# Optimization experiments

Hardware: AMD Instinct MI355X
Metric: run time of the kernel (lower is better)

Reference implementation:

```python
import jax, jax.numpy as jnp
import numpy as np

N, E, D, H, C, L = 100000, 1280000, 64, 4, 16, 3  # nodes, edges, dim, heads, head_dim, layers
NEG_SLOPE = 0.2
LN_EPS = 1e-5


def setup_inputs() -> dict:
    key = jax.random.key(0)
    ks = jax.random.split(key, 6)
    scale = 1.0 / np.sqrt(D)
    x = jax.random.normal(ks[0], (N, D), dtype=jnp.float32)
    edge_index = jax.random.randint(ks[1], (2, E), 0, N, dtype=jnp.int64)
    Wl = jax.random.normal(ks[2], (L, D, H * C), dtype=jnp.float32) * scale  # lin_l (source)
    Wr = jax.random.normal(ks[3], (L, D, H * C), dtype=jnp.float32) * scale  # lin_r (target)
    att = jax.random.normal(ks[4], (L, H, C), dtype=jnp.float32) * scale
    bias = jnp.zeros((L, H * C), dtype=jnp.float32)
    gamma = jnp.ones((L, D), dtype=jnp.float32)
    beta = jnp.zeros((L, D), dtype=jnp.float32)
    return dict(x=x, edge_index=edge_index, Wl=Wl, Wr=Wr, att=att, bias=bias, gamma=gamma, beta=beta)


def _gatv2_conv(x, src, dst, Wl, Wr, att, bias):
    # GATv2Conv (concat=True, share_weights=False, negative_slope=0.2)
    n = x.shape[0]
    xl = (x @ Wl).reshape(n, H, C)  # messages from source nodes
    xr = (x @ Wr).reshape(n, H, C)  # target-side transform
    m = xl[src] + xr[dst]  # [E', H, C]
    e = jnp.einsum('ehc,hc->eh', jax.nn.leaky_relu(m, NEG_SLOPE), att)  # [E', H]
    emax = jax.ops.segment_max(e, dst, num_segments=n)
    p = jnp.exp(e - emax[dst])
    denom = jax.ops.segment_sum(p, dst, num_segments=n)
    alpha = p / denom[dst]  # self-loops guarantee denom > 0
    out = jax.ops.segment_sum(alpha[:, :, None] * xl[src], dst, num_segments=n)  # [N, H, C]
    return out.reshape(n, H * C) + bias


def _layernorm(x, gamma, beta):
    mu = jnp.mean(x, axis=-1, keepdims=True)
    var = jnp.mean(jnp.square(x - mu), axis=-1, keepdims=True)
    return (x - mu) * jax.lax.rsqrt(var + LN_EPS) * gamma + beta


def reference(x, edge_index, Wl, Wr, att, bias, gamma, beta):
    n = x.shape[0]
    loops = jnp.arange(n, dtype=edge_index.dtype)
    src = jnp.concatenate([edge_index[0], loops])  # PyG add_self_loops=True
    dst = jnp.concatenate([edge_index[1], loops])
    for i in range(L):
        x_res = x
        x = _gatv2_conv(x, src, dst, Wl[i], Wr[i], att[i], bias[i])
        x = x + x_res  # residual
        x = _layernorm(x, gamma[i], beta[i])
        x = jax.nn.gelu(x, approximate=False)
    return x
```

## Files before the change

kernel.cpp:

```cpp
#include <hip/hip_runtime.h>
#include <math.h>


#define SCAN_CHUNK 1024

typedef __attribute__((ext_vector_type(8))) short short8;
typedef __attribute__((ext_vector_type(4))) float f32x4;

static inline int cdiv(int a, int b) { return (a + b - 1) / b; }

__device__ __forceinline__ unsigned short bf16_rtn(float v) {
    unsigned u = __float_as_uint(v);
    return (unsigned short)((u + 0x7fffu + ((u >> 16) & 1u)) >> 16);
}


__global__ void csr_init(const unsigned int* __restrict__ ei, int* __restrict__ flag,
                         int* __restrict__ deg, int N) {
    int i = blockIdx.x * blockDim.x + threadIdx.x;
    if (i < N) deg[i] = 1;
    if (blockIdx.x == 0 && threadIdx.x < 64) {
        int nz = (ei[2 * threadIdx.x + 1] != 0u) ? 1 : 0;
        unsigned long long b = __ballot(nz);
        if (threadIdx.x == 0) *flag = (b == 0ull) ? 1 : 0;
    }
}

__global__ void hist_kernel(const int* __restrict__ ei, int E, const int* __restrict__ flag,
                            int* __restrict__ deg, int* __restrict__ pos) {
    int e = blockIdx.x * blockDim.x + threadIdx.x;
    if (e >= E) return;
    int is64 = *flag;
    int d = is64 ? ei[2 * (E + e)] : ei[E + e];
    pos[e] = atomicAdd(&deg[d], 1);
}

__global__ void scan_blocks(const int* __restrict__ deg, int* __restrict__ rowptr,
                            int* __restrict__ partials, int N) {
    __shared__ int sdata[256];
    int t = threadIdx.x;
    int idx0 = blockIdx.x * SCAN_CHUNK + t * 4;
    int v[4]; int sum = 0;
    #pragma unroll
    for (int i = 0; i < 4; ++i) {
        int ii = idx0 + i;
        v[i] = (ii < N) ? deg[ii] : 0;
        sum += v[i];
    }
    sdata[t] = sum;
    __syncthreads();
    for (int off = 1; off < 256; off <<= 1) {
        int val = 0;
        if (t >= off) val = sdata[t - off];
        __syncthreads();
        if (t >= off) sdata[t] += val;
        __syncthreads();
    }
    int run = (t > 0) ? sdata[t - 1] : 0;
    #pragma unroll
    for (int i = 0; i < 4; ++i) {
        int ii = idx0 + i;
        if (ii < N) rowptr[ii] = run;
        run += v[i];
    }
    if (t == 255) partials[blockIdx.x] = sdata[255];
}

__global__ void scan_partials_k(int* __restrict__ partials, int NB) {
    __shared__ int sd[256];
    int t = threadIdx.x;
    sd[t] = (t < NB) ? partials[t] : 0;
    __syncthreads();
    for (int off = 1; off < 256; off <<= 1) {
        int val = 0;
        if (t >= off) val = sd[t - off];
        __syncthreads();
        if (t >= off) sd[t] += val;
        __syncthreads();
    }
    if (t < NB) partials[t] = (t > 0) ? sd[t - 1] : 0;
}

__global__ void add_offsets(int* __restrict__ rowptr, const int* __restrict__ partials,
                            int N, int Etot) {
    int i = blockIdx.x * blockDim.x + threadIdx.x;
    if (i < N) rowptr[i] += partials[i / SCAN_CHUNK];
    if (i == 0) rowptr[N] = Etot;
}

__global__ void fill_csr(const int* __restrict__ ei, int E, int N, const int* __restrict__ flag,
                         const int* __restrict__ rowptr, const int* __restrict__ pos,
                         int* __restrict__ col) {
    int i = blockIdx.x * blockDim.x + threadIdx.x;
    int Etot = E + N;
    if (i >= Etot + 8) return;
    if (i >= Etot) { col[Etot + (i - Etot)] = 0; return; }
    if (i < E) {
        int is64 = *flag;
        int s = is64 ? ei[2 * i] : ei[i];
        int d = is64 ? ei[2 * (E + i)] : ei[E + i];
        col[rowptr[d] + pos[i]] = s;
    } else {
        int nn = i - E;
        col[rowptr[nn]] = nn;
    }
}

__global__ void wprep_kernel(const float* __restrict__ Wl, const float* __restrict__ Wr,
                             unsigned short* __restrict__ Bh, int Lnum) {
    int t = blockIdx.x * blockDim.x + threadIdx.x;
    int total = Lnum * 2 * 4 * 2 * 64 * 8;
    if (t >= total) return;
    int j    = t & 7;
    int lane = (t >> 3) & 63;
    int kc   = (t >> 9) & 1;
    int ct   = (t >> 10) & 3;
    int h    = (t >> 12) & 1;
    int l    = t >> 13;
    const float* W = (h ? Wr : Wl) + (size_t)l * 4096;
    int k = kc * 32 + (lane >> 4) * 8 + j;
    int c = ct * 16 + (lane & 15);
    Bh[t] = bf16_rtn(W[k * 64 + c]);
}

__global__ __launch_bounds__(256) void transform_mfma(
    const float* __restrict__ x, const unsigned short* __restrict__ Bh,
    float* __restrict__ XL, float* __restrict__ XR, int N) {
    __shared__ float stage[4][16 * 68];
    int lane = threadIdx.x & 63;
    int wv = threadIdx.x >> 6;
    int wid = (blockIdx.x * blockDim.x + threadIdx.x) >> 6;
    int nw = (gridDim.x * blockDim.x) >> 6;

    const short8* Bh8 = (const short8*)Bh;
    short8 bh[8][2];
    #pragma unroll
    for (int ct = 0; ct < 8; ++ct)
        #pragma unroll
        for (int kc = 0; kc < 2; ++kc)
            bh[ct][kc] = Bh8[(ct * 2 + kc) * 64 + lane];

    int r16 = lane & 15, kq = lane >> 4;
    int ngroups = N >> 4;
    float* sbuf = stage[wv];

    for (int gidx = wid; gidx < ngroups; gidx += nw) {
        int n0 = gidx << 4;
        const float4* row = (const float4*)(x + (size_t)(n0 + r16) * 64);
        float4 f0 = row[2 * kq], f1 = row[2 * kq + 1];
        float4 f2 = row[8 + 2 * kq], f3 = row[8 + 2 * kq + 1];
        float fa[8] = {f0.x, f0.y, f0.z, f0.w, f1.x, f1.y, f1.z, f1.w};
        float fb[8] = {f2.x, f2.y, f2.z, f2.w, f3.x, f3.y, f3.z, f3.w};
        short8 ah0, ah1, al0, al1;
        #pragma unroll
        for (int j = 0; j < 8; ++j) {
            unsigned short h0 = bf16_rtn(fa[j]);
            unsigned short h1 = bf16_rtn(fb[j]);
            ah0[j] = (short)h0;
            ah1[j] = (short)h1;
            al0[j] = (short)bf16_rtn(fa[j] - __uint_as_float((unsigned)h0 << 16));
            al1[j] = (short)bf16_rtn(fb[j] - __uint_as_float((unsigned)h1 << 16));
        }

        f32x4 acc[8] = {};
        #pragma unroll
        for (int ct = 0; ct < 8; ++ct) {
            acc[ct] = __builtin_amdgcn_mfma_f32_16x16x32_bf16(ah0, bh[ct][0], acc[ct], 0, 0, 0);
            acc[ct] = __builtin_amdgcn_mfma_f32_16x16x32_bf16(ah1, bh[ct][1], acc[ct], 0, 0, 0);
            acc[ct] = __builtin_amdgcn_mfma_f32_16x16x32_bf16(al0, bh[ct][0], acc[ct], 0, 0, 0);
            acc[ct] = __builtin_amdgcn_mfma_f32_16x16x32_bf16(al1, bh[ct][1], acc[ct], 0, 0, 0);
        }
        #pragma unroll
        for (int half = 0; half < 2; ++half) {
            #pragma unroll
            for (int ct = 0; ct < 4; ++ct)
                #pragma unroll
                for (int r = 0; r < 4; ++r)
                    sbuf[(kq * 4 + r) * 68 + ct * 16 + r16] = acc[half * 4 + ct][r];
            float4* dst4 = (float4*)((half ? XR : XL) + (size_t)n0 * 64);
            #pragma unroll
            for (int w = 0; w < 4; ++w) {
                int rr = w * 4 + kq;
                float4 v = ((const float4*)sbuf)[rr * 17 + r16];
                dst4[rr * 16 + r16] = v;
            }
        }
    }
}

__global__ __launch_bounds__(512) void gat_gather_kernel(
    const float* __restrict__ XL, const float* __restrict__ XR,
    const float* __restrict__ x_res,
    const int* __restrict__ rowptr, const int* __restrict__ col,
    const float* __restrict__ att, const float* __restrict__ bias,
    const float* __restrict__ gamma, const float* __restrict__ beta,
    float* __restrict__ x_out, int N) {
    int wid = (blockIdx.x * blockDim.x + threadIdx.x) >> 6;
    if (wid >= N) return;
    int lane = threadIdx.x & 63;
    int g = lane >> 4;
    int c = lane & 15;
    const int n = wid;

    float4 xr = ((const float4*)(XR + (size_t)n * 64))[c];
    float4 av = ((const float4*)att)[c];
    int start = rowptr[n], end = rowptr[n + 1];
    const float4* XL4 = (const float4*)XL;

    float s = 0.f;
    float o0 = 0.f, o1 = 0.f, o2 = 0.f, o3 = 0.f;

    for (int k0 = start; k0 < end; k0 += 8) {
        int ka = k0 + g;
        int kb = ka + 4;
        int sa = col[ka];
        int sb = col[kb];
        float4 va = XL4[sa * 16 + c];
        float4 vb = XL4[sb * 16 + c];
        float ta0 = va.x + xr.x; ta0 = fmaxf(ta0, 0.2f * ta0);
        float ta1 = va.y + xr.y; ta1 = fmaxf(ta1, 0.2f * ta1);
        float ta2 = va.z + xr.z; ta2 = fmaxf(ta2, 0.2f * ta2);
        float ta3 = va.w + xr.w; ta3 = fmaxf(ta3, 0.2f * ta3);
        float tb0 = vb.x + xr.x; tb0 = fmaxf(tb0, 0.2f * tb0);
        float tb1 = vb.y + xr.y; tb1 = fmaxf(tb1, 0.2f * tb1);
        float tb2 = vb.z + xr.z; tb2 = fmaxf(tb2, 0.2f * tb2);
        float tb3 = vb.w + xr.w; tb3 = fmaxf(tb3, 0.2f * tb3);
        float wa = ta0 * av.x;
        wa = fmaf(ta1, av.y, wa);
        wa = fmaf(ta2, av.z, wa);
        wa = fmaf(ta3, av.w, wa);
        float wb = tb0 * av.x;
        wb = fmaf(tb1, av.y, wb);
        wb = fmaf(tb2, av.z, wb);
        wb = fmaf(tb3, av.w, wb);
        wa += __shfl_xor(wa, 1);
        wa += __shfl_xor(wa, 2);
        wb += __shfl_xor(wb, 1);
        wb += __shfl_xor(wb, 2);
        wa = (ka < end) ? wa : -1e30f;
        wb = (kb < end) ? wb : -1e30f;
        float pa = __expf(wa);
        float pb = __expf(wb);
        s += pa + pb;
        o0 = fmaf(pa, va.x, o0); o0 = fmaf(pb, vb.x, o0);
        o1 = fmaf(pa, va.y, o1); o1 = fmaf(pb, vb.y, o1);
        o2 = fmaf(pa, va.z, o2); o2 = fmaf(pb, vb.z, o2);
        o3 = fmaf(pa, va.w, o3); o3 = fmaf(pb, vb.w, o3);
    }

    #pragma unroll
    for (int mask = 16; mask <= 32; mask <<= 1) {
        s  += __shfl_xor(s, mask);
        o0 += __shfl_xor(o0, mask);
        o1 += __shfl_xor(o1, mask);
        o2 += __shfl_xor(o2, mask);
        o3 += __shfl_xor(o3, mask);
    }

    int srcLane = lane >> 2;
    int j = lane & 3;
    float o0t = __shfl(o0, srcLane);
    float o1t = __shfl(o1, srcLane);
    float o2t = __shfl(o2, srcLane);
    float o3t = __shfl(o3, srcLane);
    float st  = __shfl(s,  srcLane);
    float ov = (j & 2) ? ((j & 1) ? o3t : o2t) : ((j & 1) ? o1t : o0t);

    float gval = ov / st + bias[lane] + x_res[(size_t)n * 64 + lane];

    float mu = gval;
    #pragma unroll
    for (int mask = 1; mask < 64; mask <<= 1) mu += __shfl_xor(mu, mask);
    mu *= (1.f / 64.f);
    float d = gval - mu;
    float vs = d * d;
    #pragma unroll
    for (int mask = 1; mask < 64; mask <<= 1) vs += __shfl_xor(vs, mask);
    float rstd = rsqrtf(vs * (1.f / 64.f) + 1e-5f);
    float y = fmaf(d * rstd, gamma[lane], beta[lane]);

    float z = 0.5f * y * (1.f + erff(y * 0.70710678118654752f));
    x_out[(size_t)n * 64 + lane] = z;
}


extern "C" void kernel_launch(void* const* d_in, const int* in_sizes, int n_in,
                              void* d_out, int out_size, void* d_ws, size_t ws_size,
                              hipStream_t stream) {
    const float* x0    = (const float*)d_in[0];
    const int*   ei    = (const int*)d_in[1];
    const float* Wl    = (const float*)d_in[2];
    const float* Wr    = (const float*)d_in[3];
    const float* att   = (const float*)d_in[4];
    const float* bias  = (const float*)d_in[5];
    const float* gamma = (const float*)d_in[6];
    const float* beta  = (const float*)d_in[7];
    float* out = (float*)d_out;

    const int N = in_sizes[0] / 64;
    const int E = in_sizes[1] / 2;
    const int Lnum = in_sizes[2] / (64 * 64);
    const int Etot = E + N;

    char* ws = (char*)d_ws;
    size_t off = 0;
    auto alloc = [&](size_t bytes) {
        void* p = ws + off;
        off = (off + bytes + 255) & ~(size_t)255;
        return p;
    };
    float* XLf    = (float*)alloc((size_t)N * 64 * 4);
    float* XR     = (float*)alloc((size_t)N * 64 * 4);
    float* XA     = (float*)alloc((size_t)N * 64 * 4);
    unsigned short* Bh = (unsigned short*)alloc((size_t)Lnum * 8192 * 2);
    int* rowptr   = (int*)alloc((size_t)(N + 1) * 4);
    int* deg      = (int*)alloc((size_t)N * 4);
    int* pos      = (int*)alloc((size_t)E * 4);
    int* partials = (int*)alloc(1024 * 4);
    int* flag     = (int*)alloc(256);
    int* col      = (int*)alloc((size_t)(Etot + 8) * 4);

    wprep_kernel<<<cdiv(Lnum * 8192, 256), 256, 0, stream>>>(Wl, Wr, Bh, Lnum);
    csr_init<<<cdiv(N, 256), 256, 0, stream>>>((const unsigned int*)ei, flag, deg, N);
    hist_kernel<<<cdiv(E, 256), 256, 0, stream>>>(ei, E, flag, deg, pos);
    int NB = cdiv(N, SCAN_CHUNK);
    scan_blocks<<<NB, 256, 0, stream>>>(deg, rowptr, partials, N);
    scan_partials_k<<<1, 256, 0, stream>>>(partials, NB);
    add_offsets<<<cdiv(N + 1, 256), 256, 0, stream>>>(rowptr, partials, N, Etot);
    fill_csr<<<cdiv(Etot + 8, 256), 256, 0, stream>>>(ei, E, N, flag, rowptr, pos, col);

    const float* xcur = x0;
    for (int l = 0; l < Lnum; ++l) {
        transform_mfma<<<512, 256, 0, stream>>>(
            xcur, Bh + (size_t)l * 8192, XLf, XR, N);
        float* xnext = (l == Lnum - 1) ? out : XA;
        gat_gather_kernel<<<cdiv(N * 64, 512), 512, 0, stream>>>(
            XLf, XR, xcur, rowptr, col,
            att + (size_t)l * 64, bias + (size_t)l * 64,
            gamma + (size_t)l * 64, beta + (size_t)l * 64,
            xnext, N);
        xcur = xnext;
    }
}
```

Measured before the change: 409.5 us.

## Store source-side features in bf16 and fuse weight prep into setup

The transform kernel now writes the source-side messages (XL) as bf16 instead of fp32, and the gather kernel loads ushort4 and widens to float. This halves the bytes of the random per-edge gathers that dominate the attention/aggregation kernel. It also merges the weight-conversion kernel into the CSR init kernel and raises the transform grid from 512 to 1568 blocks. The cost is reduced precision of the messages and attention logits, which could exceed tolerance.

```diff
diff --git a/kernel.cpp b/kernel.cpp
--- a/kernel.cpp
+++ b/kernel.cpp
@@ -14,9 +14,10 @@
     return (unsigned short)((u + 0x7fffu + ((u >> 16) & 1u)) >> 16);
 }
 
-
-__global__ void csr_init(const unsigned int* __restrict__ ei, int* __restrict__ flag,
-                         int* __restrict__ deg, int N) {
+__global__ void setup_kernel(const unsigned int* __restrict__ ei, int* __restrict__ flag,
+                             int* __restrict__ deg, int N,
+                             const float* __restrict__ Wl, const float* __restrict__ Wr,
+                             unsigned short* __restrict__ Bh, int Lnum) {
     int i = blockIdx.x * blockDim.x + threadIdx.x;
     if (i < N) deg[i] = 1;
     if (blockIdx.x == 0 && threadIdx.x < 64) {
@@ -24,7 +25,22 @@
         unsigned long long b = __ballot(nz);
         if (threadIdx.x == 0) *flag = (b == 0ull) ? 1 : 0;
     }
-}
+    int total = Lnum * 2 * 4 * 2 * 64 * 8;
+    if (i < total) {
+        int t = i;
+        int j    = t & 7;
+        int lane = (t >> 3) & 63;
+        int kc   = (t >> 9) & 1;
+        int ct   = (t >> 10) & 3;
+        int h    = (t >> 12) & 1;
+        int l    = t >> 13;
+        const float* W = (h ? Wr : Wl) + (size_t)l * 4096;
+        int k = kc * 32 + (lane >> 4) * 8 + j;
+        int c = ct * 16 + (lane & 15);
+        Bh[t] = bf16_rtn(W[k * 64 + c]);
+    }
+}
+
 
 __global__ void hist_kernel(const int* __restrict__ ei, int E, const int* __restrict__ flag,
                             int* __restrict__ deg, int* __restrict__ pos) {
@@ -106,26 +122,9 @@
     }
 }
 
-__global__ void wprep_kernel(const float* __restrict__ Wl, const float* __restrict__ Wr,
-                             unsigned short* __restrict__ Bh, int Lnum) {
-    int t = blockIdx.x * blockDim.x + threadIdx.x;
-    int total = Lnum * 2 * 4 * 2 * 64 * 8;
-    if (t >= total) return;
-    int j    = t & 7;
-    int lane = (t >> 3) & 63;
-    int kc   = (t >> 9) & 1;
-    int ct   = (t >> 10) & 3;
-    int h    = (t >> 12) & 1;
-    int l    = t >> 13;
-    const float* W = (h ? Wr : Wl) + (size_t)l * 4096;
-    int k = kc * 32 + (lane >> 4) * 8 + j;
-    int c = ct * 16 + (lane & 15);
-    Bh[t] = bf16_rtn(W[k * 64 + c]);
-}
-
 __global__ __launch_bounds__(256) void transform_mfma(
     const float* __restrict__ x, const unsigned short* __restrict__ Bh,
-    float* __restrict__ XL, float* __restrict__ XR, int N) {
+    unsigned short* __restrict__ XL, float* __restrict__ XR, int N) {
     __shared__ float stage[4][16 * 68];
     int lane = threadIdx.x & 63;
     int wv = threadIdx.x >> 6;
@@ -170,26 +169,41 @@
             acc[ct] = __builtin_amdgcn_mfma_f32_16x16x32_bf16(al0, bh[ct][0], acc[ct], 0, 0, 0);
             acc[ct] = __builtin_amdgcn_mfma_f32_16x16x32_bf16(al1, bh[ct][1], acc[ct], 0, 0, 0);
         }
-        #pragma unroll
-        for (int half = 0; half < 2; ++half) {
+
+        #pragma unroll
+        for (int ct = 0; ct < 4; ++ct)
             #pragma unroll
-            for (int ct = 0; ct < 4; ++ct)
-                #pragma unroll
-                for (int r = 0; r < 4; ++r)
-                    sbuf[(kq * 4 + r) * 68 + ct * 16 + r16] = acc[half * 4 + ct][r];
-            float4* dst4 = (float4*)((half ? XR : XL) + (size_t)n0 * 64);
+            for (int r = 0; r < 4; ++r)
+                sbuf[(kq * 4 + r) * 68 + ct * 16 + r16] = acc[ct][r];
+        #pragma unroll
+        for (int w = 0; w < 4; ++w) {
+            int rr = w * 4 + kq;
+            float4 v = ((const float4*)sbuf)[rr * 17 + r16];
+            ushort4 hv;
+            hv.x = bf16_rtn(v.x);
+            hv.y = bf16_rtn(v.y);
+            hv.z = bf16_rtn(v.z);
+            hv.w = bf16_rtn(v.w);
+            ((ushort4*)(XL + (size_t)(n0 + rr) * 64))[r16] = hv;
+        }
+
+        #pragma unroll
+        for (int ct = 0; ct < 4; ++ct)
             #pragma unroll
-            for (int w = 0; w < 4; ++w) {
-                int rr = w * 4 + kq;
-                float4 v = ((const float4*)sbuf)[rr * 17 + r16];
-                dst4[rr * 16 + r16] = v;
-            }
+            for (int r = 0; r < 4; ++r)
+                sbuf[(kq * 4 + r) * 68 + ct * 16 + r16] = acc[4 + ct][r];
+        float4* dst4 = (float4*)(XR + (size_t)n0 * 64);
+        #pragma unroll
+        for (int w = 0; w < 4; ++w) {
+            int rr = w * 4 + kq;
+            float4 v = ((const float4*)sbuf)[rr * 17 + r16];
+            dst4[rr * 16 + r16] = v;
         }
     }
 }
 
 __global__ __launch_bounds__(512) void gat_gather_kernel(
-    const float* __restrict__ XL, const float* __restrict__ XR,
+    const unsigned short* __restrict__ XL, const float* __restrict__ XR,
     const float* __restrict__ x_res,
     const int* __restrict__ rowptr, const int* __restrict__ col,
     const float* __restrict__ att, const float* __restrict__ bias,
@@ -205,7 +219,7 @@
     float4 xr = ((const float4*)(XR + (size_t)n * 64))[c];
     float4 av = ((const float4*)att)[c];
     int start = rowptr[n], end = rowptr[n + 1];
-    const float4* XL4 = (const float4*)XL;
+    const ushort4* XL4 = (const ushort4*)XL;
 
     float s = 0.f;
     float o0 = 0.f, o1 = 0.f, o2 = 0.f, o3 = 0.f;
@@ -215,16 +229,24 @@
         int kb = ka + 4;
         int sa = col[ka];
         int sb = col[kb];
-        float4 va = XL4[sa * 16 + c];
-        float4 vb = XL4[sb * 16 + c];
-        float ta0 = va.x + xr.x; ta0 = fmaxf(ta0, 0.2f * ta0);
-        float ta1 = va.y + xr.y; ta1 = fmaxf(ta1, 0.2f * ta1);
-        float ta2 = va.z + xr.z; ta2 = fmaxf(ta2, 0.2f * ta2);
-        float ta3 = va.w + xr.w; ta3 = fmaxf(ta3, 0.2f * ta3);
-        float tb0 = vb.x + xr.x; tb0 = fmaxf(tb0, 0.2f * tb0);
-        float tb1 = vb.y + xr.y; tb1 = fmaxf(tb1, 0.2f * tb1);
-        float tb2 = vb.z + xr.z; tb2 = fmaxf(tb2, 0.2f * tb2);
-        float tb3 = vb.w + xr.w; tb3 = fmaxf(tb3, 0.2f * tb3);
+        ushort4 ha = XL4[(size_t)sa * 16 + c];
+        ushort4 hb = XL4[(size_t)sb * 16 + c];
+        float va0 = __uint_as_float((unsigned)ha.x << 16);
+        float va1 = __uint_as_float((unsigned)ha.y << 16);
+        float va2 = __uint_as_float((unsigned)ha.z << 16);
+        float va3 = __uint_as_float((unsigned)ha.w << 16);
+        float vb0 = __uint_as_float((unsigned)hb.x << 16);
+        float vb1 = __uint_as_float((unsigned)hb.y << 16);
+        float vb2 = __uint_as_float((unsigned)hb.z << 16);
+        float vb3 = __uint_as_float((unsigned)hb.w << 16);
+        float ta0 = va0 + xr.x; ta0 = fmaxf(ta0, 0.2f * ta0);
+        float ta1 = va1 + xr.y; ta1 = fmaxf(ta1, 0.2f * ta1);
+        float ta2 = va2 + xr.z; ta2 = fmaxf(ta2, 0.2f * ta2);
+        float ta3 = va3 + xr.w; ta3 = fmaxf(ta3, 0.2f * ta3);
+        float tb0 = vb0 + xr.x; tb0 = fmaxf(tb0, 0.2f * tb0);
+        float tb1 = vb1 + xr.y; tb1 = fmaxf(tb1, 0.2f * tb1);
+        float tb2 = vb2 + xr.z; tb2 = fmaxf(tb2, 0.2f * tb2);
+        float tb3 = vb3 + xr.w; tb3 = fmaxf(tb3, 0.2f * tb3);
         float wa = ta0 * av.x;
         wa = fmaf(ta1, av.y, wa);
         wa = fmaf(ta2, av.z, wa);
@@ -242,10 +264,10 @@
         float pa = __expf(wa);
         float pb = __expf(wb);
         s += pa + pb;
-        o0 = fmaf(pa, va.x, o0); o0 = fmaf(pb, vb.x, o0);
-        o1 = fmaf(pa, va.y, o1); o1 = fmaf(pb, vb.y, o1);
-        o2 = fmaf(pa, va.z, o2); o2 = fmaf(pb, vb.z, o2);
-        o3 = fmaf(pa, va.w, o3); o3 = fmaf(pb, vb.w, o3);
+        o0 = fmaf(pa, va0, o0); o0 = fmaf(pb, vb0, o0);
+        o1 = fmaf(pa, va1, o1); o1 = fmaf(pb, vb1, o1);
+        o2 = fmaf(pa, va2, o2); o2 = fmaf(pb, vb2, o2);
+        o3 = fmaf(pa, va3, o3); o3 = fmaf(pb, vb3, o3);
     }
 
     #pragma unroll
@@ -309,7 +331,7 @@
         off = (off + bytes + 255) & ~(size_t)255;
         return p;
     };
-    float* XLf    = (float*)alloc((size_t)N * 64 * 4);
+    unsigned short* XLb = (unsigned short*)alloc((size_t)N * 64 * 2);
     float* XR     = (float*)alloc((size_t)N * 64 * 4);
     float* XA     = (float*)alloc((size_t)N * 64 * 4);
     unsigned short* Bh = (unsigned short*)alloc((size_t)Lnum * 8192 * 2);
@@ -320,8 +342,8 @@
     int* flag     = (int*)alloc(256);
     int* col      = (int*)alloc((size_t)(Etot + 8) * 4);
 
-    wprep_kernel<<<cdiv(Lnum * 8192, 256), 256, 0, stream>>>(Wl, Wr, Bh, Lnum);
-    csr_init<<<cdiv(N, 256), 256, 0, stream>>>((const unsigned int*)ei, flag, deg, N);
+    setup_kernel<<<cdiv(N, 256), 256, 0, stream>>>((const unsigned int*)ei, flag, deg, N,
+                                                   Wl, Wr, Bh, Lnum);
     hist_kernel<<<cdiv(E, 256), 256, 0, stream>>>(ei, E, flag, deg, pos);
     int NB = cdiv(N, SCAN_CHUNK);
     scan_blocks<<<NB, 256, 0, stream>>>(deg, rowptr, partials, N);
@@ -331,11 +353,11 @@
 
     const float* xcur = x0;
     for (int l = 0; l < Lnum; ++l) {
-        transform_mfma<<<512, 256, 0, stream>>>(
-            xcur, Bh + (size_t)l * 8192, XLf, XR, N);
+        transform_mfma<<<1568, 256, 0, stream>>>(
+            xcur, Bh + (size_t)l * 8192, XLb, XR, N);
         float* xnext = (l == Lnum - 1) ? out : XA;
         gat_gather_kernel<<<cdiv(N * 64, 512), 512, 0, stream>>>(
-            XLf, XR, xcur, rowptr, col,
+            XLb, XR, xcur, rowptr, col,
             att + (size_t)l * 64, bias + (size_t)l * 64,
             gamma + (size_t)l * 64, beta + (size_t)l * 64,
             xnext, N);
```

Measured after the change: 398.2 us. 1.03x faster.
